# Kernel optimization log

Hardware: AMD Instinct MI355X
Metric: run time of the kernel (lower is better)

Reference implementation:

```python
import jax, jax.numpy as jnp
import numpy as np

N = 100000   # nodes
E = 1600000  # edges
F = 128      # num_features
NF = 4       # n_factor
D = 64       # n_dim = dim // n_factor = 256 // 4
NL = 3       # n_layer
G = 128      # num graphs in batch


def setup_inputs() -> dict:
    key = jax.random.key(0)
    ks = jax.random.split(key, 10)
    s = 0.05
    x = jax.random.normal(ks[0], (N, F), jnp.float32)
    edge_index = jax.random.randint(ks[1], (2, E), 0, N)
    att = jax.random.uniform(ks[2], (NF, E), jnp.float32)
    batch = jnp.sort(jax.random.randint(ks[3], (N,), 0, G))
    lin_W = jax.random.normal(ks[4], (NF, F, D), jnp.float32) * s
    lin_b = jnp.zeros((NF, D), jnp.float32)
    conv_Wrel = jax.random.normal(ks[5], (NF, NL, D, D), jnp.float32) * s
    conv_brel = jnp.zeros((NF, NL, D), jnp.float32)
    conv_Wroot = jax.random.normal(ks[6], (NF, NL, D, D), jnp.float32) * s
    gru_Wih = jax.random.normal(ks[7], (NF, 3 * D, D), jnp.float32) * s
    gru_Whh = jax.random.normal(ks[8], (NF, 3 * D, D), jnp.float32) * s
    gru_bih = jnp.zeros((NF, 3 * D), jnp.float32)
    gru_bhh = jnp.zeros((NF, 3 * D), jnp.float32)
    return dict(x=x, edge_index=edge_index, att=att, batch=batch,
                lin_W=lin_W, lin_b=lin_b,
                conv_Wrel=conv_Wrel, conv_brel=conv_brel, conv_Wroot=conv_Wroot,
                gru_Wih=gru_Wih, gru_Whh=gru_Whh, gru_bih=gru_bih, gru_bhh=gru_bhh,
                num_graphs=G)


def _gru_cell(xin, h, Wih, Whh, bih, bhh):
    # torch.nn.GRU single step: r,z,n gates
    gi = xin @ Wih.T + bih  # [N, 3D]
    gh = h @ Whh.T + bhh
    ir, iz, inn = jnp.split(gi, 3, axis=-1)
    hr, hz, hn = jnp.split(gh, 3, axis=-1)
    r = jax.nn.sigmoid(ir + hr)
    z = jax.nn.sigmoid(iz + hz)
    n = jnp.tanh(inn + r * hn)
    return (1.0 - z) * n + z * h


def reference(x, edge_index, att, batch, lin_W, lin_b, conv_Wrel, conv_brel,
              conv_Wroot, gru_Wih, gru_Whh, gru_bih, gru_bhh, num_graphs):
    src, dst = edge_index[0], edge_index[1]
    counts = jax.ops.segment_sum(jnp.ones((N,), x.dtype), batch, num_segments=num_graphs)
    counts = jnp.maximum(counts, 1.0)[:, None]
    outs, feats = [], []
    for f in range(NF):
        w = att[f][:, None]                       # [E,1] edge weights for this factor
        out = x @ lin_W[f] + lin_b[f]             # [N,D]
        h = out                                   # initial GRU hidden state
        for l in range(NL):
            # GraphConv: lin_rel(scatter_add(w * x_src -> dst)) + lin_root(x)
            agg = jax.ops.segment_sum(out[src] * w, dst, num_segments=N)
            m = jax.nn.relu(agg @ conv_Wrel[f, l] + conv_brel[f, l] + out @ conv_Wroot[f, l])
            h = _gru_cell(m, h, gru_Wih[f], gru_Whh[f], gru_bih[f], gru_bhh[f])
            out = h
        feats.append(out)
        # global mean pool
        outs.append(jax.ops.segment_sum(out, batch, num_segments=num_graphs) / counts)
    return (jnp.stack(outs), jnp.stack(feats))
```

## Files before the change

### kernel.cpp

```cpp
#include <hip/hip_runtime.h>

#define NN   100000
#define EE   1600000
#define FDIM 128
#define NFAC 4
#define DD   64
#define NLAY 3
#define GG   128


#define PF_STRIDE 57344
#define OFF_WREL  8192
#define OFF_WROOT 20480
#define OFF_WIH   32768
#define OFF_WHH   45056
#define PREP_TOTAL (NFAC * PF_STRIDE)

typedef __bf16 bf16x8_t __attribute__((ext_vector_type(8)));
typedef float  f32x4_t  __attribute__((ext_vector_type(4)));

__device__ __forceinline__ unsigned short f2bf(float x) {
    unsigned u = __float_as_uint(x);
    u += 0x7fffu + ((u >> 16) & 1u);
    return (unsigned short)(u >> 16);
}
__device__ __forceinline__ float b2f(unsigned short h) {
    return __uint_as_float(((unsigned)h) << 16);
}
__device__ __forceinline__ float sigm(float x) { return 1.f / (1.f + __expf(-x)); }
__device__ __forceinline__ float tanh_f(float x) {
    float t = __expf(-2.f * fabsf(x));
    float r = (1.f - t) / (1.f + t);
    return x >= 0.f ? r : -r;
}

__global__ __launch_bounds__(256) void k_init(int* deg, int* cursor, float* outs) {
    int i = blockIdx.x * 256 + threadIdx.x;
    if (i < NN) { deg[i] = 0; cursor[i] = 0; }
    if (i < NFAC * GG * DD) outs[i] = 0.f;
}

__global__ __launch_bounds__(256) void k_prep(const float* x, const float* linW,
                                              const float* wrel, const float* wroot,
                                              const float* wih, const float* whh,
                                              unsigned short* x16, unsigned short* prep) {
    for (int i = blockIdx.x * 256 + threadIdx.x; i < NN * FDIM; i += gridDim.x * 256)
        x16[i] = f2bf(x[i]);
    for (int idx = blockIdx.x * 256 + threadIdx.x; idx < PREP_TOTAL; idx += gridDim.x * 256) {
        int f = idx / PF_STRIDE, r = idx % PF_STRIDE;
        int e, KB, mode, l = 0;
        if (r < OFF_WREL)       { e = r;                 KB = 4; mode = 0; }
        else if (r < OFF_WROOT) { int rr = r - OFF_WREL;  l = rr >> 12; e = rr & 4095; KB = 2; mode = 1; }
        else if (r < OFF_WIH)   { int rr = r - OFF_WROOT; l = rr >> 12; e = rr & 4095; KB = 2; mode = 2; }
        else if (r < OFF_WHH)   { e = r - OFF_WIH;        KB = 2; mode = 3; }
        else                    { e = r - OFF_WHH;        KB = 2; mode = 4; }
        int j = e & 7, lane = (e >> 3) & 63, t = e >> 9;
        int kb = t % KB, nt = t / KB;
        int k = kb * 32 + (lane >> 4) * 8 + j;
        int n = nt * 16 + (lane & 15);
        float v;
        if (mode == 0)      v = linW[(f * FDIM + k) * DD + n];
        else if (mode == 1) v = wrel[((f * 3 + l) * DD + k) * DD + n];
        else if (mode == 2) v = wroot[((f * 3 + l) * DD + k) * DD + n];
        else if (mode == 3) v = wih[(f * 192 + n) * DD + k];
        else                v = whh[(f * 192 + n) * DD + k];
        prep[idx] = f2bf(v);
    }
}

__global__ __launch_bounds__(256) void k_count(const int* batch, float* counts) {
    __shared__ int lb[GG + 1];
    int t = threadIdx.x;
    if (t <= GG) {
        int lo = 0, hi = NN;
        while (lo < hi) { int mid = (lo + hi) >> 1; if (batch[mid] < t) lo = mid + 1; else hi = mid; }
        lb[t] = lo;
    }
    __syncthreads();
    if (t < GG) counts[t] = (float)(lb[t + 1] - lb[t]);
}

__global__ __launch_bounds__(256) void k_deg(const int* ei, int* deg) {
    int e = blockIdx.x * 256 + threadIdx.x;
    if (e < EE) atomicAdd(&deg[ei[EE + e]], 1);
}
__global__ __launch_bounds__(256) void k_scan1(const int* deg, int* row_pos, int* bsum) {
    __shared__ int lds[256];
    int tid = threadIdx.x, idx = blockIdx.x * 256 + tid;
    int v = (idx < NN) ? deg[idx] : 0;
    lds[tid] = v; __syncthreads();
    for (int s = 1; s < 256; s <<= 1) {
        int t = (tid >= s) ? lds[tid - s] : 0;
        __syncthreads();
        lds[tid] += t;
        __syncthreads();
    }
    if (idx < NN) row_pos[idx] = lds[tid] - v;
    if (tid == 255) bsum[blockIdx.x] = lds[255];
}
__global__ __launch_bounds__(512) void k_scan2(int* bsum) {
    __shared__ int lds[512];
    int tid = threadIdx.x;
    int v = (tid < 391) ? bsum[tid] : 0;
    lds[tid] = v; __syncthreads();
    for (int s = 1; s < 512; s <<= 1) {
        int t = (tid >= s) ? lds[tid - s] : 0;
        __syncthreads();
        lds[tid] += t;
        __syncthreads();
    }
    bsum[tid] = lds[tid] - v;
}
__global__ __launch_bounds__(256) void k_rowptr(const int* row_pos, const int* boff, int* row_ptr) {
    int i = blockIdx.x * 256 + threadIdx.x;
    if (i < NN) row_ptr[i] = row_pos[i] + boff[i >> 8];
    if (i == 0) row_ptr[NN] = EE;
}
__global__ __launch_bounds__(256) void k_fill(const int* ei, const float* att,
                                              const int* row_ptr, int* cursor,
                                              int* csr_src, float* csr_att) {
    int e = blockIdx.x * 256 + threadIdx.x;
    if (e >= EE) return;
    int d = ei[EE + e];
    int slot = row_ptr[d] + atomicAdd(&cursor[d], 1);
    csr_src[slot] = ei[e];
    *(float4*)(csr_att + (size_t)slot * 4) =
        make_float4(att[e], att[EE + e], att[2 * EE + e], att[3 * EE + e]);
}
__global__ __launch_bounds__(256) void k_att(const float* csr_att, float* att_t) {
    int e = blockIdx.x * 256 + threadIdx.x;
    if (e >= EE) return;
    float4 v = *(const float4*)(csr_att + (size_t)e * 4);
    att_t[e]                  = v.x;
    att_t[(size_t)EE + e]     = v.y;
    att_t[(size_t)2 * EE + e] = v.z;
    att_t[(size_t)3 * EE + e] = v.w;
}

__global__ __launch_bounds__(256) void k_lin(const unsigned short* x16, const unsigned short* prep,
                                             const float* linb, unsigned short* out16) {
    int n0 = blockIdx.x * 64;
    __shared__ unsigned short xs[64 * 136];
    int tid = threadIdx.x;
    for (int t = tid; t < 1024; t += 256) {
        int row = t >> 4, seg = t & 15;
        int gn = n0 + row; if (gn >= NN) gn = NN - 1;
        *(uint4*)(xs + row * 136 + seg * 8) = *(const uint4*)(x16 + (size_t)gn * FDIM + seg * 8);
    }
    __syncthreads();
    int w = tid >> 6, lane = tid & 63, mrow = lane & 15, q = lane >> 4;
    const unsigned short* wp = prep + w * PF_STRIDE;
    bf16x8_t a[4][4];
#pragma unroll
    for (int mt = 0; mt < 4; mt++)
#pragma unroll
        for (int kb = 0; kb < 4; kb++)
            a[mt][kb] = *(const bf16x8_t*)(xs + (mt * 16 + mrow) * 136 + kb * 32 + q * 8);
#pragma unroll
    for (int nt = 0; nt < 4; nt++) {
        bf16x8_t b[4];
#pragma unroll
        for (int kb = 0; kb < 4; kb++)
            b[kb] = *(const bf16x8_t*)(wp + ((nt * 4 + kb) * 64 + lane) * 8);
        int col = nt * 16 + mrow;
        float bias = linb[w * DD + col];
#pragma unroll
        for (int mt = 0; mt < 4; mt++) {
            f32x4_t acc = {0.f, 0.f, 0.f, 0.f};
#pragma unroll
            for (int kb = 0; kb < 4; kb++)
                acc = __builtin_amdgcn_mfma_f32_16x16x32_bf16(a[mt][kb], b[kb], acc, 0, 0, 0);
#pragma unroll
            for (int r = 0; r < 4; r++) {
                int node = n0 + mt * 16 + q * 4 + r;
                if (node < NN) out16[((size_t)w * NN + node) * DD + col] = f2bf(acc[r] + bias);
            }
        }
    }
}

__global__ __launch_bounds__(256) void k_gather(const int* row_ptr, const int* csr_src, const float* att_t,
                                                const unsigned short* in16, unsigned short* agg16) {
    int tid = threadIdx.x, f = blockIdx.y;
    int grp = tid >> 4, d4 = tid & 15;
    int n = blockIdx.x * 16 + grp;
    int row = row_ptr[n], end = row_ptr[n + 1];
    int total = end - row;
    const unsigned short* inf = in16 + (size_t)f * NN * DD;
    const float* attf = att_t + (size_t)f * EE;
    float a0 = 0.f, a1 = 0.f, a2 = 0.f, a3 = 0.f;
    for (int base = 0; base < total; base += 8) {
        int s[8]; float w[8];
#pragma unroll
        for (int j = 0; j < 8; j++) {
            int e = base + j;
            int idx = row + (e < total ? e : total - 1);
            s[j] = csr_src[idx];
            float ww = attf[idx];
            w[j] = (e < total) ? ww : 0.f;
        }
        uint2 v[8];
#pragma unroll
        for (int j = 0; j < 8; j++)
            v[j] = *(const uint2*)(inf + (size_t)s[j] * DD + d4 * 4);
#pragma unroll
        for (int j = 0; j < 8; j++) {
            a0 = fmaf(w[j], __uint_as_float(v[j].x << 16), a0);
            a1 = fmaf(w[j], __uint_as_float(v[j].x & 0xffff0000u), a1);
            a2 = fmaf(w[j], __uint_as_float(v[j].y << 16), a2);
            a3 = fmaf(w[j], __uint_as_float(v[j].y & 0xffff0000u), a3);
        }
    }
    ushort4 r;
    r.x = f2bf(a0); r.y = f2bf(a1); r.z = f2bf(a2); r.w = f2bf(a3);
    *(ushort4*)(agg16 + ((size_t)f * NN + n) * DD + d4 * 4) = r;
}

__global__ __launch_bounds__(256) void k_layer(int l, const unsigned short* agg16, unsigned short* out16,
                                               const unsigned short* prep, const float* brel,
                                               const float* bih, const float* bhh,
                                               float* feats, int last) {
    int f = blockIdx.y, n0 = blockIdx.x * 64;
    __shared__ unsigned short A1[64 * 72];
    __shared__ unsigned short A2[64 * 72];
    __shared__ unsigned short Mt[64 * 72];
    int tid = threadIdx.x;
    const unsigned short* aggf = agg16 + (size_t)f * NN * DD;
    const unsigned short* outf = out16 + (size_t)f * NN * DD;
    for (int t = tid; t < 512; t += 256) {
        int row = t >> 3, seg = t & 7;
        int gn = n0 + row; if (gn >= NN) gn = NN - 1;
        *(uint4*)(A1 + row * 72 + seg * 8) = *(const uint4*)(aggf + (size_t)gn * DD + seg * 8);
        *(uint4*)(A2 + row * 72 + seg * 8) = *(const uint4*)(outf + (size_t)gn * DD + seg * 8);
    }
    __syncthreads();
    int w = tid >> 6, lane = tid & 63, mrow = lane & 15, q = lane >> 4;
    const unsigned short* wrel  = prep + f * PF_STRIDE + OFF_WREL  + l * 4096;
    const unsigned short* wroot = prep + f * PF_STRIDE + OFF_WROOT + l * 4096;

    {
        bf16x8_t wr1[2], wr2[2];
#pragma unroll
        for (int kb = 0; kb < 2; kb++) {
            wr1[kb] = *(const bf16x8_t*)(wrel  + ((w * 2 + kb) * 64 + lane) * 8);
            wr2[kb] = *(const bf16x8_t*)(wroot + ((w * 2 + kb) * 64 + lane) * 8);
        }
        int col = w * 16 + mrow;
        float bias = brel[(f * 3 + l) * DD + col];
#pragma unroll
        for (int mt = 0; mt < 4; mt++) {
            f32x4_t acc = {0.f, 0.f, 0.f, 0.f};
#pragma unroll
            for (int kb = 0; kb < 2; kb++) {
                bf16x8_t a1 = *(const bf16x8_t*)(A1 + (mt * 16 + mrow) * 72 + kb * 32 + q * 8);
                acc = __builtin_amdgcn_mfma_f32_16x16x32_bf16(a1, wr1[kb], acc, 0, 0, 0);
                bf16x8_t a2 = *(const bf16x8_t*)(A2 + (mt * 16 + mrow) * 72 + kb * 32 + q * 8);
                acc = __builtin_amdgcn_mfma_f32_16x16x32_bf16(a2, wr2[kb], acc, 0, 0, 0);
            }
#pragma unroll
            for (int r = 0; r < 4; r++) {
                float mv = acc[r] + bias;
                mv = mv > 0.f ? mv : 0.f;
                Mt[(mt * 16 + q * 4 + r) * 72 + col] = f2bf(mv);
            }
        }
    }
    __syncthreads();

    const unsigned short* wih = prep + f * PF_STRIDE + OFF_WIH;
    const unsigned short* whh = prep + f * PF_STRIDE + OFF_WHH;
    bf16x8_t Br[2], Bz[2], Bn[2], Cr[2], Cz[2], Cn[2];
#pragma unroll
    for (int kb = 0; kb < 2; kb++) {
        Br[kb] = *(const bf16x8_t*)(wih + (((w)     * 2 + kb) * 64 + lane) * 8);
        Bz[kb] = *(const bf16x8_t*)(wih + (((w + 4) * 2 + kb) * 64 + lane) * 8);
        Bn[kb] = *(const bf16x8_t*)(wih + (((w + 8) * 2 + kb) * 64 + lane) * 8);
        Cr[kb] = *(const bf16x8_t*)(whh + (((w)     * 2 + kb) * 64 + lane) * 8);
        Cz[kb] = *(const bf16x8_t*)(whh + (((w + 4) * 2 + kb) * 64 + lane) * 8);
        Cn[kb] = *(const bf16x8_t*)(whh + (((w + 8) * 2 + kb) * 64 + lane) * 8);
    }
    int col = w * 16 + mrow;
    float bi_r = bih[f * 192 + col],        bh_r = bhh[f * 192 + col];
    float bi_z = bih[f * 192 + 64 + col],   bh_z = bhh[f * 192 + 64 + col];
    float bi_n = bih[f * 192 + 128 + col],  bh_n = bhh[f * 192 + 128 + col];
    unsigned short* outwf = out16 + (size_t)f * NN * DD;
#pragma unroll
    for (int mt = 0; mt < 4; mt++) {
        f32x4_t ir = {0.f,0.f,0.f,0.f}, iz = {0.f,0.f,0.f,0.f}, in_ = {0.f,0.f,0.f,0.f};
        f32x4_t hr = {0.f,0.f,0.f,0.f}, hz = {0.f,0.f,0.f,0.f}, hn  = {0.f,0.f,0.f,0.f};
#pragma unroll
        for (int kb = 0; kb < 2; kb++) {
            bf16x8_t am = *(const bf16x8_t*)(Mt + (mt * 16 + mrow) * 72 + kb * 32 + q * 8);
            bf16x8_t ah = *(const bf16x8_t*)(A2 + (mt * 16 + mrow) * 72 + kb * 32 + q * 8);
            ir  = __builtin_amdgcn_mfma_f32_16x16x32_bf16(am, Br[kb], ir, 0, 0, 0);
            iz  = __builtin_amdgcn_mfma_f32_16x16x32_bf16(am, Bz[kb], iz, 0, 0, 0);
            in_ = __builtin_amdgcn_mfma_f32_16x16x32_bf16(am, Bn[kb], in_, 0, 0, 0);
            hr  = __builtin_amdgcn_mfma_f32_16x16x32_bf16(ah, Cr[kb], hr, 0, 0, 0);
            hz  = __builtin_amdgcn_mfma_f32_16x16x32_bf16(ah, Cz[kb], hz, 0, 0, 0);
            hn  = __builtin_amdgcn_mfma_f32_16x16x32_bf16(ah, Cn[kb], hn, 0, 0, 0);
        }
#pragma unroll
        for (int r = 0; r < 4; r++) {
            float rg = sigm(ir[r] + bi_r + hr[r] + bh_r);
            float z  = sigm(iz[r] + bi_z + hz[r] + bh_z);
            float nn = tanh_f(in_[r] + bi_n + rg * (hn[r] + bh_n));
            float h  = b2f(A2[(mt * 16 + q * 4 + r) * 72 + col]);
            float hp = (1.f - z) * nn + z * h;
            int node = n0 + mt * 16 + q * 4 + r;
            if (node < NN) {
                outwf[(size_t)node * DD + col] = f2bf(hp);
                if (last) feats[((size_t)f * NN + node) * DD + col] = hp;
            }
        }
    }
}

__global__ __launch_bounds__(256) void k_pool(const float* feats, const int* batch, float* outs) {
    int f = blockIdx.y, w = threadIdx.x >> 6, lane = threadIdx.x & 63;
    int nbase = blockIdx.x * 256 + w * 64;
    if (nbase >= NN) return;
    int g_cur = batch[nbase];
    float acc = 0.f;
    for (int i = 0; i < 64; i++) {
        int n = nbase + i;
        if (n >= NN) break;
        int g = batch[n];
        float v = feats[((size_t)f * NN + n) * DD + lane];
        if (g != g_cur) {
            atomicAdd(&outs[(f * GG + g_cur) * DD + lane], acc);
            acc = v; g_cur = g;
        } else acc += v;
    }
    atomicAdd(&outs[(f * GG + g_cur) * DD + lane], acc);
}
__global__ __launch_bounds__(256) void k_norm(float* outs, const float* counts) {
    int i = blockIdx.x * 256 + threadIdx.x;
    if (i < NFAC * GG * DD) {
        int g = (i >> 6) & (GG - 1);
        outs[i] /= fmaxf(counts[g], 1.f);
    }
}

extern "C" void kernel_launch(void* const* d_in, const int* in_sizes, int n_in,
                              void* d_out, int out_size, void* d_ws, size_t ws_size,
                              hipStream_t stream) {
    const float* x    = (const float*)d_in[0];
    const int*   ei   = (const int*)d_in[1];
    const float* att  = (const float*)d_in[2];
    const int*   batch= (const int*)d_in[3];
    const float* linW = (const float*)d_in[4];
    const float* linb = (const float*)d_in[5];
    const float* wrel = (const float*)d_in[6];
    const float* brel = (const float*)d_in[7];
    const float* wroot= (const float*)d_in[8];
    const float* wih  = (const float*)d_in[9];
    const float* whh  = (const float*)d_in[10];
    const float* bih  = (const float*)d_in[11];
    const float* bhh  = (const float*)d_in[12];

    float* outs  = (float*)d_out;
    float* feats = (float*)d_out + NFAC * GG * DD;

    char* p = (char*)d_ws;
    unsigned short* out16 = (unsigned short*)p; p += (size_t)NFAC * NN * DD * 2;
    unsigned short* agg16 = (unsigned short*)p; p += (size_t)NFAC * NN * DD * 2;
    unsigned short* x16   = (unsigned short*)p; p += (size_t)NN * FDIM * 2;
    unsigned short* prep  = (unsigned short*)p; p += (size_t)PREP_TOTAL * 2;
    float* att_t          = (float*)p;          p += (size_t)EE * 16;
    int* csr_src          = (int*)p;            p += (size_t)EE * 4;
    int* deg              = (int*)p;            p += (size_t)NN * 4;
    int* cursor           = (int*)p;            p += (size_t)NN * 4;
    int* row_pos          = (int*)p;            p += (size_t)NN * 4;
    int* row_ptr          = (int*)p;            p += (size_t)(NN + 1) * 4;
    int* boff             = (int*)p;            p += 512 * 4;
    float* counts         = (float*)p;          p += 512;

    float* csr_att = (float*)agg16;

    k_init  <<<dim3(391),  dim3(256), 0, stream>>>(deg, cursor, outs);
    k_prep  <<<dim3(4096), dim3(256), 0, stream>>>(x, linW, wrel, wroot, wih, whh, x16, prep);
    k_count <<<dim3(1),    dim3(256), 0, stream>>>(batch, counts);
    k_deg   <<<dim3(6250), dim3(256), 0, stream>>>(ei, deg);
    k_scan1 <<<dim3(391),  dim3(256), 0, stream>>>(deg, row_pos, boff);
    k_scan2 <<<dim3(1),    dim3(512), 0, stream>>>(boff);
    k_rowptr<<<dim3(391),  dim3(256), 0, stream>>>(row_pos, boff, row_ptr);
    k_fill  <<<dim3(6250), dim3(256), 0, stream>>>(ei, att, row_ptr, cursor, csr_src, csr_att);
    k_att   <<<dim3(6250), dim3(256), 0, stream>>>(csr_att, att_t);
    k_lin   <<<dim3(1563), dim3(256), 0, stream>>>(x16, prep, linb, out16);
    for (int l = 0; l < NLAY; l++) {
        k_gather<<<dim3(6250, 4), dim3(256), 0, stream>>>(row_ptr, csr_src, att_t, out16, agg16);
        k_layer <<<dim3(1563, 4), dim3(256), 0, stream>>>(l, agg16, out16, prep, brel, bih, bhh,
                                                          feats, (l == NLAY - 1) ? 1 : 0);
    }
    k_pool <<<dim3(391, 4), dim3(256), 0, stream>>>(feats, batch, outs);
    k_norm <<<dim3(128),    dim3(256), 0, stream>>>(outs, counts);
}
```

Before: 988.5 us.

## Split each node's edge list across four lane groups in gather with shuffle reduction

The gather kernel now assigns one 64-lane wavefront per node instead of 16 lanes. Four 16-lane subgroups each process a different edge, two edges per iteration, and the partial sums are combined with cross-lane shuffles before one subgroup writes the result. The aim is more memory-level parallelism per node and less serialization on high-degree nodes. In exchange it launches four times more blocks, removes the 8-deep per-thread load batching, adds shuffle-reduction overhead, and wastes lanes on low-degree nodes.

New measurement: 1.121 ms. 1.13x slower.

```diff
diff --git a/kernel.cpp b/kernel.cpp
--- a/kernel.cpp
+++ b/kernel.cpp
@@ -182,38 +182,57 @@
 __global__ __launch_bounds__(256) void k_gather(const int* row_ptr, const int* csr_src, const float* att_t,
                                                 const unsigned short* in16, unsigned short* agg16) {
     int tid = threadIdx.x, f = blockIdx.y;
-    int grp = tid >> 4, d4 = tid & 15;
-    int n = blockIdx.x * 16 + grp;
+    int lane = tid & 63, es = lane >> 4, d4 = lane & 15;
+    int n = blockIdx.x * 4 + (tid >> 6);
     int row = row_ptr[n], end = row_ptr[n + 1];
     int total = end - row;
     const unsigned short* inf = in16 + (size_t)f * NN * DD;
     const float* attf = att_t + (size_t)f * EE;
     float a0 = 0.f, a1 = 0.f, a2 = 0.f, a3 = 0.f;
-    for (int base = 0; base < total; base += 8) {
-        int s[8]; float w[8];
-#pragma unroll
-        for (int j = 0; j < 8; j++) {
-            int e = base + j;
-            int idx = row + (e < total ? e : total - 1);
-            s[j] = csr_src[idx];
-            float ww = attf[idx];
-            w[j] = (e < total) ? ww : 0.f;
-        }
-        uint2 v[8];
-#pragma unroll
-        for (int j = 0; j < 8; j++)
-            v[j] = *(const uint2*)(inf + (size_t)s[j] * DD + d4 * 4);
-#pragma unroll
-        for (int j = 0; j < 8; j++) {
-            a0 = fmaf(w[j], __uint_as_float(v[j].x << 16), a0);
-            a1 = fmaf(w[j], __uint_as_float(v[j].x & 0xffff0000u), a1);
-            a2 = fmaf(w[j], __uint_as_float(v[j].y << 16), a2);
-            a3 = fmaf(w[j], __uint_as_float(v[j].y & 0xffff0000u), a3);
-        }
-    }
-    ushort4 r;
-    r.x = f2bf(a0); r.y = f2bf(a1); r.z = f2bf(a2); r.w = f2bf(a3);
-    *(ushort4*)(agg16 + ((size_t)f * NN + n) * DD + d4 * 4) = r;
+    int full = total & ~7;
+    int base = 0;
+    for (; base < full; base += 8) {
+        int i0 = row + base + es, i1 = i0 + 4;
+        int s0 = csr_src[i0], s1 = csr_src[i1];
+        float w0 = attf[i0], w1 = attf[i1];
+        uint2 v0 = *(const uint2*)(inf + (size_t)(unsigned)s0 * DD + d4 * 4);
+        uint2 v1 = *(const uint2*)(inf + (size_t)(unsigned)s1 * DD + d4 * 4);
+        a0 = fmaf(w0, __uint_as_float(v0.x << 16), a0);
+        a1 = fmaf(w0, __uint_as_float(v0.x & 0xffff0000u), a1);
+        a2 = fmaf(w0, __uint_as_float(v0.y << 16), a2);
+        a3 = fmaf(w0, __uint_as_float(v0.y & 0xffff0000u), a3);
+        a0 = fmaf(w1, __uint_as_float(v1.x << 16), a0);
+        a1 = fmaf(w1, __uint_as_float(v1.x & 0xffff0000u), a1);
+        a2 = fmaf(w1, __uint_as_float(v1.y << 16), a2);
+        a3 = fmaf(w1, __uint_as_float(v1.y & 0xffff0000u), a3);
+    }
+    if (base < total) {
+        int j0 = base + es, j1 = base + es + 4;
+        int i0 = row + (j0 < total ? j0 : total - 1);
+        int i1 = row + (j1 < total ? j1 : total - 1);
+        int s0 = csr_src[i0], s1 = csr_src[i1];
+        float w0 = (j0 < total) ? attf[i0] : 0.f;
+        float w1 = (j1 < total) ? attf[i1] : 0.f;
+        uint2 v0 = *(const uint2*)(inf + (size_t)(unsigned)s0 * DD + d4 * 4);
+        uint2 v1 = *(const uint2*)(inf + (size_t)(unsigned)s1 * DD + d4 * 4);
+        a0 = fmaf(w0, __uint_as_float(v0.x << 16), a0);
+        a1 = fmaf(w0, __uint_as_float(v0.x & 0xffff0000u), a1);
+        a2 = fmaf(w0, __uint_as_float(v0.y << 16), a2);
+        a3 = fmaf(w0, __uint_as_float(v0.y & 0xffff0000u), a3);
+        a0 = fmaf(w1, __uint_as_float(v1.x << 16), a0);
+        a1 = fmaf(w1, __uint_as_float(v1.x & 0xffff0000u), a1);
+        a2 = fmaf(w1, __uint_as_float(v1.y << 16), a2);
+        a3 = fmaf(w1, __uint_as_float(v1.y & 0xffff0000u), a3);
+    }
+    a0 += __shfl_xor(a0, 16); a1 += __shfl_xor(a1, 16);
+    a2 += __shfl_xor(a2, 16); a3 += __shfl_xor(a3, 16);
+    a0 += __shfl_xor(a0, 32); a1 += __shfl_xor(a1, 32);
+    a2 += __shfl_xor(a2, 32); a3 += __shfl_xor(a3, 32);
+    if (es == 0) {
+        ushort4 r;
+        r.x = f2bf(a0); r.y = f2bf(a1); r.z = f2bf(a2); r.w = f2bf(a3);
+        *(ushort4*)(agg16 + ((size_t)f * NN + n) * DD + d4 * 4) = r;
+    }
 }
 
 __global__ __launch_bounds__(256) void k_layer(int l, const unsigned short* agg16, unsigned short* out16,
@@ -388,7 +407,7 @@
     k_att   <<<dim3(6250), dim3(256), 0, stream>>>(csr_att, att_t);
     k_lin   <<<dim3(1563), dim3(256), 0, stream>>>(x16, prep, linb, out16);
     for (int l = 0; l < NLAY; l++) {
-        k_gather<<<dim3(6250, 4), dim3(256), 0, stream>>>(row_ptr, csr_src, att_t, out16, agg16);
+        k_gather<<<dim3(25000, 4), dim3(256), 0, stream>>>(row_ptr, csr_src, att_t, out16, agg16);
         k_layer <<<dim3(1563, 4), dim3(256), 0, stream>>>(l, agg16, out16, prep, brel, bih, bhh,
                                                           feats, (l == NLAY - 1) ? 1 : 0);
     }
```

## Sort nodes by in-degree via counting sort to balance gather work

Applied to the files above, without the earlier changes.

Adds a degree histogram, scan and permutation pass that orders destination nodes by in-degree, and makes the gather kernel process nodes in that order. Each block's 16 node groups then see similar edge counts, which is meant to cut intra-block divergence and tail imbalance in the gather loop. The cost is three extra small kernels plus an indirection per node. Neighbouring nodes no longer share a block, so the agg writes and row_ptr reads become scattered.

New measurement: 1.302 ms. 1.32x slower.

```diff
diff --git a/kernel.cpp b/kernel.cpp
--- a/kernel.cpp
+++ b/kernel.cpp
@@ -34,10 +34,11 @@
     return x >= 0.f ? r : -r;
 }
 
-__global__ __launch_bounds__(256) void k_init(int* deg, int* cursor, float* outs) {
+__global__ __launch_bounds__(256) void k_init(int* deg, int* cursor, float* outs, int* hist) {
     int i = blockIdx.x * 256 + threadIdx.x;
     if (i < NN) { deg[i] = 0; cursor[i] = 0; }
     if (i < NFAC * GG * DD) outs[i] = 0.f;
+    if (i < 256) hist[i] = 0;
 }
 
 __global__ __launch_bounds__(256) void k_prep(const float* x, const float* linW,
@@ -137,6 +138,37 @@
     att_t[(size_t)3 * EE + e] = v.w;
 }
 
+__global__ __launch_bounds__(256) void k_hist(const int* deg, int* hist) {
+    __shared__ int lh[256];
+    int tid = threadIdx.x;
+    lh[tid] = 0; __syncthreads();
+    int i = blockIdx.x * 256 + tid;
+    if (i < NN) { int b = deg[i]; if (b > 255) b = 255; atomicAdd(&lh[b], 1); }
+    __syncthreads();
+    if (lh[tid]) atomicAdd(&hist[tid], lh[tid]);
+}
+__global__ __launch_bounds__(256) void k_hscan(int* hist, int* hcur) {
+    __shared__ int lds[256];
+    int tid = threadIdx.x;
+    int v = hist[tid];
+    lds[tid] = v; __syncthreads();
+    for (int s = 1; s < 256; s <<= 1) {
+        int t = (tid >= s) ? lds[tid - s] : 0;
+        __syncthreads();
+        lds[tid] += t;
+        __syncthreads();
+    }
+    hist[tid] = lds[tid] - v;
+    hcur[tid] = 0;
+}
+__global__ __launch_bounds__(256) void k_perm(const int* deg, const int* hist, int* hcur, int* perm) {
+    int i = blockIdx.x * 256 + threadIdx.x;
+    if (i >= NN) return;
+    int b = deg[i]; if (b > 255) b = 255;
+    int pos = hist[b] + atomicAdd(&hcur[b], 1);
+    perm[pos] = i;
+}
+
 __global__ __launch_bounds__(256) void k_lin(const unsigned short* x16, const unsigned short* prep,
                                              const float* linb, unsigned short* out16) {
     int n0 = blockIdx.x * 64;
@@ -179,11 +211,12 @@
     }
 }
 
-__global__ __launch_bounds__(256) void k_gather(const int* row_ptr, const int* csr_src, const float* att_t,
+__global__ __launch_bounds__(256) void k_gather(const int* perm, const int* row_ptr,
+                                                const int* csr_src, const float* att_t,
                                                 const unsigned short* in16, unsigned short* agg16) {
     int tid = threadIdx.x, f = blockIdx.y;
     int grp = tid >> 4, d4 = tid & 15;
-    int n = blockIdx.x * 16 + grp;
+    int n = perm[blockIdx.x * 16 + grp];
     int row = row_ptr[n], end = row_ptr[n + 1];
     int total = end - row;
     const unsigned short* inf = in16 + (size_t)f * NN * DD;
@@ -372,12 +405,15 @@
     int* cursor           = (int*)p;            p += (size_t)NN * 4;
     int* row_pos          = (int*)p;            p += (size_t)NN * 4;
     int* row_ptr          = (int*)p;            p += (size_t)(NN + 1) * 4;
+    int* perm             = (int*)p;            p += (size_t)NN * 4;
     int* boff             = (int*)p;            p += 512 * 4;
+    int* hist             = (int*)p;            p += 256 * 4;
+    int* hcur             = (int*)p;            p += 256 * 4;
     float* counts         = (float*)p;          p += 512;
 
     float* csr_att = (float*)agg16;
 
-    k_init  <<<dim3(391),  dim3(256), 0, stream>>>(deg, cursor, outs);
+    k_init  <<<dim3(391),  dim3(256), 0, stream>>>(deg, cursor, outs, hist);
     k_prep  <<<dim3(4096), dim3(256), 0, stream>>>(x, linW, wrel, wroot, wih, whh, x16, prep);
     k_count <<<dim3(1),    dim3(256), 0, stream>>>(batch, counts);
     k_deg   <<<dim3(6250), dim3(256), 0, stream>>>(ei, deg);
@@ -386,9 +422,12 @@
     k_rowptr<<<dim3(391),  dim3(256), 0, stream>>>(row_pos, boff, row_ptr);
     k_fill  <<<dim3(6250), dim3(256), 0, stream>>>(ei, att, row_ptr, cursor, csr_src, csr_att);
     k_att   <<<dim3(6250), dim3(256), 0, stream>>>(csr_att, att_t);
+    k_hist  <<<dim3(391),  dim3(256), 0, stream>>>(deg, hist);
+    k_hscan <<<dim3(1),    dim3(256), 0, stream>>>(hist, hcur);
+    k_perm  <<<dim3(391),  dim3(256), 0, stream>>>(deg, hist, hcur, perm);
     k_lin   <<<dim3(1563), dim3(256), 0, stream>>>(x16, prep, linb, out16);
     for (int l = 0; l < NLAY; l++) {
-        k_gather<<<dim3(6250, 4), dim3(256), 0, stream>>>(row_ptr, csr_src, att_t, out16, agg16);
+        k_gather<<<dim3(6250, 4), dim3(256), 0, stream>>>(perm, row_ptr, csr_src, att_t, out16, agg16);
         k_layer <<<dim3(1563, 4), dim3(256), 0, stream>>>(l, agg16, out16, prep, brel, bih, bhh,
                                                           feats, (l == NLAY - 1) ? 1 : 0);
     }
```
